# Performance work log

Hardware: AMD Instinct MI355X
Metric: run time of the kernel (lower is better)

## Reference

```python
import jax, jax.numpy as jnp
import numpy as np

B, M, L, HID, H, LAYERS = 16, 128, 512, 256, 4, 2
DH = HID // H  # 64 = head dim, also kernel_param dim


def _ln(x, g, b, eps=1e-5):
    mu = jnp.mean(x, axis=-1, keepdims=True)
    var = jnp.mean((x - mu) ** 2, axis=-1, keepdims=True)
    return (x - mu) / jnp.sqrt(var + eps) * g + b


def setup_inputs() -> dict:
    key = jax.random.key(0)
    ks = jax.random.split(key, 24)
    s = 0.05
    return {
        "ct_t": jax.random.uniform(ks[0], (B, M), jnp.float32),
        "ts_t": jax.random.uniform(ks[1], (B, L), jnp.float32),
        "ct_emb": jax.random.normal(ks[2], (B, M, HID), jnp.float32),
        "ts_emb": jax.random.normal(ks[3], (B, L, HID), jnp.float32),
        "kernel_param": jax.random.normal(ks[4], (DH,), jnp.float32),
        "ct_W": jax.random.normal(ks[5], (HID, HID), jnp.float32) * s,
        "ct_b": jnp.zeros((HID,), jnp.float32),
        "fW0": jax.random.normal(ks[6], (HID, HID), jnp.float32) * s,
        "fb0": jnp.zeros((HID,), jnp.float32),
        "fW1": jax.random.normal(ks[7], (HID, HID), jnp.float32) * s,
        "fb1": jnp.zeros((HID,), jnp.float32),
        "fW2": jax.random.normal(ks[8], (HID, HID), jnp.float32) * s,
        "fb2": jnp.zeros((HID,), jnp.float32),
        "f_ln_g": jnp.ones((HID,), jnp.float32),
        "f_ln_b": jnp.zeros((HID,), jnp.float32),
        "Wqkv": jax.random.normal(ks[9], (LAYERS, 3 * HID, HID), jnp.float32) * s,
        "bqkv": jnp.zeros((LAYERS, 3 * HID), jnp.float32),
        "Wo": jax.random.normal(ks[10], (LAYERS, HID, HID), jnp.float32) * s,
        "bo": jnp.zeros((LAYERS, HID), jnp.float32),
        "W1": jax.random.normal(ks[11], (LAYERS, 2 * HID, HID), jnp.float32) * s,
        "b1": jnp.zeros((LAYERS, 2 * HID), jnp.float32),
        "W2": jax.random.normal(ks[12], (LAYERS, HID, 2 * HID), jnp.float32) * s,
        "b2": jnp.zeros((LAYERS, HID), jnp.float32),
        "ln1_g": jnp.ones((LAYERS, HID), jnp.float32),
        "ln1_b": jnp.zeros((LAYERS, HID), jnp.float32),
        "ln2_g": jnp.ones((LAYERS, HID), jnp.float32),
        "ln2_b": jnp.zeros((LAYERS, HID), jnp.float32),
        "pred_W": jax.random.normal(ks[13], (1, HID), jnp.float32) * s,
        "pred_b": jnp.zeros((1,), jnp.float32),
    }


def reference(ct_t, ts_t, ct_emb, ts_emb, kernel_param, ct_W, ct_b,
              fW0, fb0, fW1, fb1, fW2, fb2, f_ln_g, f_ln_b,
              Wqkv, bqkv, Wo, bo, W1, b1, W2, b2,
              ln1_g, ln1_b, ln2_g, ln2_b, pred_W, pred_b):
    # --- TN tokenizer: multi-scale RBF kernel temporal fusion ---
    alpha = jax.nn.softplus(kernel_param)                       # [DH]  log(1+exp(p))
    ct_e = (jnp.einsum('bmd,ed->bme', ct_emb, ct_W) + ct_b)     # [B,M,HID]
    ct_e = ct_e.reshape(B, M, H, DH)
    diff = ct_t[:, :, None] - ts_t[:, None, :]                  # [B,M,L]
    norm = (diff * diff)[..., None]                             # [B,M,L,1]
    outs = []
    for s in range(H):                                          # fixed small loop over scales
        z = (-float(s)) * alpha * norm                          # [B,M,L,DH]
        w = jax.nn.logsumexp(z, axis=3, keepdims=True)          # [B,M,L,1]
        sim = jnp.exp(z - w)                                    # normalized kernel sims
        outs.append(jnp.einsum('bmnd,bmd->bnd', sim, ct_e[:, :, s, :]))  # scatter over ts events
    temp = jnp.concatenate(outs, axis=-1)                       # [B,L,HID]
    # --- Fusion module ---
    aux = jax.nn.elu(temp @ fW0.T + fb0 + ts_emb @ fW1.T + fb1)
    x = _ln(aux @ fW2.T + fb2 + ts_emb, f_ln_g, f_ln_b)         # [B,L,HID]
    # --- Transformer encoder (post-LN, gelu, no dropout at eval) ---
    inv_sqrt = 1.0 / np.sqrt(DH).astype(np.float32)
    for l in range(LAYERS):
        qkv = x @ Wqkv[l].T + bqkv[l]                           # [B,L,3*HID]
        q, k, v = jnp.split(qkv, 3, axis=-1)
        def heads(t):
            return t.reshape(B, L, H, DH).transpose(0, 2, 1, 3)
        q, k, v = heads(q), heads(k), heads(v)
        att = jax.nn.softmax(jnp.einsum('bhqd,bhkd->bhqk', q, k) * inv_sqrt, axis=-1)
        o = jnp.einsum('bhqk,bhkd->bhqd', att, v).transpose(0, 2, 1, 3).reshape(B, L, HID)
        x = _ln(x + o @ Wo[l].T + bo[l], ln1_g[l], ln1_b[l])
        ff = jax.nn.gelu(x @ W1[l].T + b1[l], approximate=False) @ W2[l].T + b2[l]
        x = _ln(x + ff, ln2_g[l], ln2_b[l])
    return x @ pred_W.T + pred_b                                # [B,L,1]
```

## Files before the change

### kernel.cpp

```cpp
#include <hip/hip_runtime.h>
#include <hip/hip_bf16.h>
#include <cstddef>

#define Bsz 16
#define Msz 128
#define Lsz 512
#define HIDs 256

typedef __attribute__((ext_vector_type(4))) float f32x4;
typedef __attribute__((ext_vector_type(8))) __bf16 bf16x8;
typedef __attribute__((ext_vector_type(8))) unsigned short ushort8;

#define CHEB_K 12
#define PI_F 3.14159265358979323846f

static __device__ inline unsigned short f2bf(float f) {
    __hip_bfloat16 h = __float2bfloat16(f);
    return *(unsigned short*)&h;
}
static __device__ inline float bf2f(unsigned short u) {
    return __builtin_bit_cast(float, (unsigned)u << 16);
}
static __device__ inline void gload16(const ushort* g, ushort* l) {
    __builtin_amdgcn_global_load_lds(
        (const __attribute__((address_space(1))) void*)g,
        (__attribute__((address_space(3))) void*)l, 16, 0, 0);
}

__global__ __launch_bounds__(256) void cvt_all_kernel(
    const float* __restrict__ ts_emb, const float* __restrict__ ct_emb,
    const float* __restrict__ ct_W, const float* __restrict__ fW0,
    const float* __restrict__ fW1, const float* __restrict__ fW2,
    const float* __restrict__ Wqkv, const float* __restrict__ Wo,
    const float* __restrict__ W1, const float* __restrict__ W2,
    ushort* __restrict__ Xcat, ushort* __restrict__ Wcat,
    ushort* __restrict__ cebin, ushort* __restrict__ wct,
    ushort* __restrict__ wf2, ushort* __restrict__ wqkv,
    ushort* __restrict__ wo, ushort* __restrict__ w1, ushort* __restrict__ w2)
{
    const unsigned u = blockIdx.x * 256u + threadIdx.x;
    const float* src; ushort* dst; unsigned rel;
    if (u < 262144u) {
        rel = u; src = ts_emb;
        dst = Xcat + ((size_t)(rel >> 5) * 512 + 256 + (rel & 31) * 8);
    } else if (u < 327680u) { rel = u - 262144u; src = ct_emb; dst = cebin + (size_t)rel * 8; }
    else if (u < 335872u) { rel = u - 327680u; src = ct_W; dst = wct + (size_t)rel * 8; }
    else if (u < 344064u) { rel = u - 335872u; src = fW0;
        dst = Wcat + ((size_t)(rel >> 5) * 512 + (rel & 31) * 8); }
    else if (u < 352256u) { rel = u - 344064u; src = fW1;
        dst = Wcat + ((size_t)(rel >> 5) * 512 + 256 + (rel & 31) * 8); }
    else if (u < 360448u) { rel = u - 352256u; src = fW2; dst = wf2 + (size_t)rel * 8; }
    else if (u < 409600u) { rel = u - 360448u; src = Wqkv; dst = wqkv + (size_t)rel * 8; }
    else if (u < 425984u) { rel = u - 409600u; src = Wo;  dst = wo + (size_t)rel * 8; }
    else if (u < 458752u) { rel = u - 425984u; src = W1;  dst = w1 + (size_t)rel * 8; }
    else                  { rel = u - 458752u; src = W2;  dst = w2 + (size_t)rel * 8; }
    float4 a = ((const float4*)src)[(size_t)rel * 2];
    float4 b = ((const float4*)src)[(size_t)rel * 2 + 1];
    ushort8 o;
    o[0] = f2bf(a.x); o[1] = f2bf(a.y); o[2] = f2bf(a.z); o[3] = f2bf(a.w);
    o[4] = f2bf(b.x); o[5] = f2bf(b.y); o[6] = f2bf(b.z); o[7] = f2bf(b.w);
    *(ushort8*)dst = o;
}

__global__ __launch_bounds__(256) void gemm_mfma_kernel(
    const ushort* __restrict__ X, const ushort* __restrict__ W,
    const float* __restrict__ bias, const float* __restrict__ bias2,
    float* __restrict__ Yf, ushort* __restrict__ Yb,
    int NR, int K, int OUT, int act)
{
    __shared__ ushort As[2][64 * 64];
    __shared__ ushort Bs[2][128 * 64];

    const int nbx = OUT >> 7;
    const int bx = blockIdx.x % nbx;
    const int by = blockIdx.x / nbx;
    const int r0 = by << 6, o0 = bx << 7;
    const int tid = threadIdx.x;
    const int w = tid >> 6;
    const int lane = tid & 63;
    const int wr = w >> 1, wc = w & 1;
    const int lr = lane & 15, lg = lane >> 4;

    const int grow = lane >> 3;
    const int gchunk = (lane & 7) ^ grow;

    unsigned aoff[2][2], boff[4][2];
    #pragma unroll
    for (int f = 0; f < 2; f++) {
        unsigned cc = (unsigned)((lg + 4 * f) ^ (lr & 7)) * 16u;
        #pragma unroll
        for (int m = 0; m < 2; m++)
            aoff[m][f] = (unsigned)(wr * 32 + m * 16 + lr) * 128u + cc;
        #pragma unroll
        for (int n = 0; n < 4; n++)
            boff[n][f] = (unsigned)(wc * 64 + n * 16 + lr) * 128u + cc;
    }

    f32x4 acc[2][4];
    #pragma unroll
    for (int m = 0; m < 2; m++)
        #pragma unroll
        for (int n = 0; n < 4; n++) acc[m][n] = (f32x4){0.f, 0.f, 0.f, 0.f};

    const int nk = K >> 6;

    auto stage = [&](int buf, int ks) {
        const int k0 = ks << 6;
        #pragma unroll
        for (int i = 0; i < 2; i++) {
            int row = w * 16 + i * 8 + grow;
            gload16(X + (size_t)(r0 + row) * K + k0 + gchunk * 8,
                    &As[buf][(w * 16 + i * 8) * 64]);
        }
        #pragma unroll
        for (int i = 0; i < 4; i++) {
            int row = w * 32 + i * 8 + grow;
            gload16(W + (size_t)(o0 + row) * K + k0 + gchunk * 8,
                    &Bs[buf][(w * 32 + i * 8) * 64]);
        }
    };

    stage(0, 0);
    __syncthreads();
    int cur = 0;
    for (int ks = 0; ks < nk; ks++) {
        if (ks + 1 < nk) stage(cur ^ 1, ks + 1);
        const char* Ab = (const char*)As[cur];
        const char* Bb = (const char*)Bs[cur];
        #pragma unroll
        for (int f = 0; f < 2; f++) {
            bf16x8 av[2], bv[4];
            #pragma unroll
            for (int m = 0; m < 2; m++)
                av[m] = *(const bf16x8*)(Ab + aoff[m][f]);
            #pragma unroll
            for (int n = 0; n < 4; n++)
                bv[n] = *(const bf16x8*)(Bb + boff[n][f]);
            #pragma unroll
            for (int m = 0; m < 2; m++)
                #pragma unroll
                for (int n = 0; n < 4; n++)
                    acc[m][n] = __builtin_amdgcn_mfma_f32_16x16x32_bf16(
                        av[m], bv[n], acc[m][n], 0, 0, 0);
        }
        __syncthreads();
        cur ^= 1;
    }

    const int ocol0 = o0 + wc * 64;
    float bn[4];
    #pragma unroll
    for (int n = 0; n < 4; n++) {
        int o = ocol0 + n * 16 + lr;
        bn[n] = bias[o] + (bias2 ? bias2[o] : 0.f);
    }

    #pragma unroll
    for (int m = 0; m < 2; m++) {
        #pragma unroll
        for (int p = 0; p < 4; p++) {
            int r = r0 + wr * 32 + m * 16 + 4 * lg + p;
            size_t rb = (size_t)r * OUT;
            #pragma unroll
            for (int n = 0; n < 4; n++) {
                int o = ocol0 + n * 16 + lr;
                float v = acc[m][n][p] + bn[n];
                if (act == 1)      v = (v > 0.f) ? v : (__expf(v) - 1.f);
                else if (act == 2) v = 0.5f * v * (1.f + erff(v * 0.70710678118654752f));
                if (Yf) Yf[rb + o] = v;
                if (Yb) Yb[rb + o] = f2bf(v);
            }
        }
    }
}

__global__ __launch_bounds__(256) void gemm_ln_kernel(
    const ushort* __restrict__ X, const ushort* __restrict__ W,
    const float* __restrict__ bias, const float* __restrict__ add,
    const float* __restrict__ lng, const float* __restrict__ lnb,
    float* __restrict__ Xf, ushort* __restrict__ Xb,
    const float* __restrict__ predW, const float* __restrict__ predb,
    float* __restrict__ pout, int K)
{
    __shared__ ushort As[2][32 * 64];
    __shared__ ushort Bs[2][256 * 64];
    __shared__ float redA[32][4];
    __shared__ float redB[32][4];

    const int r0 = blockIdx.x << 5;
    const int tid = threadIdx.x;
    const int w = tid >> 6;
    const int lane = tid & 63;
    const int lr = lane & 15, lg = lane >> 4;
    const int grow = lane >> 3;
    const int gchunk = (lane & 7) ^ grow;

    unsigned aoff[2][2], boff[4][2];
    #pragma unroll
    for (int f = 0; f < 2; f++) {
        unsigned cc = (unsigned)((lg + 4 * f) ^ (lr & 7)) * 16u;
        #pragma unroll
        for (int m = 0; m < 2; m++)
            aoff[m][f] = (unsigned)(m * 16 + lr) * 128u + cc;
        #pragma unroll
        for (int n = 0; n < 4; n++)
            boff[n][f] = (unsigned)(w * 64 + n * 16 + lr) * 128u + cc;
    }

    f32x4 acc[2][4];
    #pragma unroll
    for (int m = 0; m < 2; m++)
        #pragma unroll
        for (int n = 0; n < 4; n++) acc[m][n] = (f32x4){0.f, 0.f, 0.f, 0.f};

    const int nk = K >> 6;

    auto stage = [&](int buf, int ks) {
        const int k0 = ks << 6;
        gload16(X + (size_t)(r0 + w * 8 + grow) * K + k0 + gchunk * 8,
                &As[buf][(w * 8) * 64]);
        #pragma unroll
        for (int i = 0; i < 8; i++) {
            gload16(W + (size_t)(w * 64 + i * 8 + grow) * K + k0 + gchunk * 8,
                    &Bs[buf][(w * 64 + i * 8) * 64]);
        }
    };

    stage(0, 0);
    __syncthreads();
    int cur = 0;
    for (int ks = 0; ks < nk; ks++) {
        if (ks + 1 < nk) stage(cur ^ 1, ks + 1);
        const char* Ab = (const char*)As[cur];
        const char* Bb = (const char*)Bs[cur];
        #pragma unroll
        for (int f = 0; f < 2; f++) {
            bf16x8 av[2], bv[4];
            #pragma unroll
            for (int m = 0; m < 2; m++)
                av[m] = *(const bf16x8*)(Ab + aoff[m][f]);
            #pragma unroll
            for (int n = 0; n < 4; n++)
                bv[n] = *(const bf16x8*)(Bb + boff[n][f]);
            #pragma unroll
            for (int m = 0; m < 2; m++)
                #pragma unroll
                for (int n = 0; n < 4; n++)
                    acc[m][n] = __builtin_amdgcn_mfma_f32_16x16x32_bf16(
                        av[m], bv[n], acc[m][n], 0, 0, 0);
        }
        __syncthreads();
        cur ^= 1;
    }

    const int col0 = w * 64;
    float bn[4], gv[4], bv2[4], pwv[4];
    #pragma unroll
    for (int n = 0; n < 4; n++) {
        int o = col0 + n * 16 + lr;
        bn[n] = bias[o];
        gv[n] = lng[o];
        bv2[n] = lnb[o];
        pwv[n] = predW ? predW[o] : 0.f;
    }
    #pragma unroll
    for (int m = 0; m < 2; m++)
        #pragma unroll
        for (int p = 0; p < 4; p++) {
            int r = r0 + m * 16 + 4 * lg + p;
            size_t rb = (size_t)r * 256;
            #pragma unroll
            for (int n = 0; n < 4; n++)
                acc[m][n][p] += bn[n] + add[rb + col0 + n * 16 + lr];
        }

    #pragma unroll
    for (int m = 0; m < 2; m++)
        #pragma unroll
        for (int p = 0; p < 4; p++) {
            float s = acc[m][0][p] + acc[m][1][p] + acc[m][2][p] + acc[m][3][p];
            #pragma unroll
            for (int o = 1; o <= 8; o <<= 1) s += __shfl_xor(s, o);
            if (lr == 0) redA[m * 16 + 4 * lg + p][w] = s;
        }
    __syncthreads();
    float mu[2][4];
    #pragma unroll
    for (int m = 0; m < 2; m++)
        #pragma unroll
        for (int p = 0; p < 4; p++) {
            int row = m * 16 + 4 * lg + p;
            mu[m][p] = (redA[row][0] + redA[row][1] + redA[row][2] + redA[row][3])
                       * (1.f / 256.f);
        }

    #pragma unroll
    for (int m = 0; m < 2; m++)
        #pragma unroll
        for (int p = 0; p < 4; p++) {
            float q = 0.f;
            #pragma unroll
            for (int n = 0; n < 4; n++) {
                float dl = acc[m][n][p] - mu[m][p];
                q = fmaf(dl, dl, q);
            }
            #pragma unroll
            for (int o = 1; o <= 8; o <<= 1) q += __shfl_xor(q, o);
            if (lr == 0) redB[m * 16 + 4 * lg + p][w] = q;
        }
    __syncthreads();

    #pragma unroll
    for (int m = 0; m < 2; m++)
        #pragma unroll
        for (int p = 0; p < 4; p++) {
            int row = m * 16 + 4 * lg + p;
            float var = (redB[row][0] + redB[row][1] + redB[row][2] + redB[row][3])
                        * (1.f / 256.f);
            float rsig = rsqrtf(var + 1e-5f);
            int r = r0 + row;
            size_t rb = (size_t)r * 256;
            float pd = 0.f;
            #pragma unroll
            for (int n = 0; n < 4; n++) {
                int o = col0 + n * 16 + lr;
                float xn = (acc[m][n][p] - mu[m][p]) * rsig * gv[n] + bv2[n];
                if (Xf) Xf[rb + o] = xn;
                if (Xb) Xb[rb + o] = f2bf(xn);
                pd = fmaf(xn, pwv[n], pd);
            }
            if (predW) {
                #pragma unroll
                for (int o = 1; o <= 8; o <<= 1) pd += __shfl_xor(pd, o);
                if (lr == 0) redA[row][w] = pd;
            }
        }
    if (predW) {
        __syncthreads();
        if (tid < 32)
            pout[r0 + tid] = redA[tid][0] + redA[tid][1] + redA[tid][2]
                           + redA[tid][3] + predb[0];
    }
}

__global__ __launch_bounds__(256) void cheb_kernel(
    const float* __restrict__ kp, float* __restrict__ clut, float* __restrict__ cD)
{
    __shared__ float costab[CHEB_K][32];
    __shared__ float xq[32];
    __shared__ float alph[64];
    const int t = threadIdx.x;
    if (t < 64) {
        float p = kp[t];
        alph[t] = fmaxf(p, 0.f) + log1pf(__expf(-fabsf(p)));
    }
    #pragma unroll
    for (int i = 0; i < 2; i++) {
        int idx = i * 256 + t;
        if (idx < CHEB_K * 32) {
            int k = idx >> 5, q = idx & 31;
            float th = (q + 0.5f) * (PI_F / 32.f);
            costab[k][q] = __cosf((float)k * th);
        }
    }
    if (t < 32) xq[t] = 0.5f * (1.f + __cosf((t + 0.5f) * (PI_F / 32.f)));
    __syncthreads();

    if (t >= 192) return;
    const int d = t & 63, s1 = t >> 6;
    const float u = (float)(s1 + 1) * alph[d];
    float f[32];
    #pragma unroll
    for (int q = 0; q < 32; q++) f[q] = __expf(-u * xq[q]);
    #pragma unroll
    for (int k = 0; k < CHEB_K; k++) {
        float sum = 0.f;
        #pragma unroll
        for (int q = 0; q < 32; q++) sum = fmaf(f[q], costab[k][q], sum);
        float c = sum * ((k == 0 ? 1.f : 2.f) / 32.f);
        clut[s1 * (CHEB_K * 64) + k * 64 + d] = c;
        float sr = c;
        #pragma unroll
        for (int o = 1; o <= 32; o <<= 1) sr += __shfl_xor(sr, o, 64);
        if (d == 0) cD[s1 * CHEB_K + k] = sr;
    }
}

__global__ __launch_bounds__(256) void denom3_kernel(
    const float* __restrict__ ct_t, const float* __restrict__ ts_t,
    const float* __restrict__ cD, ushort* __restrict__ invW)
{
    __shared__ float cd[3][CHEB_K];
    const int tid = threadIdx.x;
    if (tid < 3 * CHEB_K) cd[tid / CHEB_K][tid % CHEB_K] = cD[tid];
    __syncthreads();

    const unsigned G = blockIdx.x * 256u + tid;
    const int b = G >> 16;
    const int n = (G >> 7) & 511;
    const int m = G & 127;

    float x = ct_t[b * Msz + m] - ts_t[b * Lsz + n];
    x = x * x;
    const float xi = 2.f * x - 1.f;
    const float xi2 = 2.f * xi;

    float t0 = 1.f, t1 = xi;
    float a1 = cd[0][0] + cd[0][1] * xi;
    float a2 = cd[1][0] + cd[1][1] * xi;
    float a3 = cd[2][0] + cd[2][1] * xi;
    #pragma unroll
    for (int k = 2; k < CHEB_K; k++) {
        float tn = fmaf(xi2, t1, -t0);
        a1 = fmaf(cd[0][k], tn, a1);
        a2 = fmaf(cd[1][k], tn, a2);
        a3 = fmaf(cd[2][k], tn, a3);
        t0 = t1; t1 = tn;
    }
    const size_t base = ((size_t)b * 3 * Lsz + n) * Msz + m;
    invW[base]                         = f2bf(1.f / a1);
    invW[base + (size_t)Lsz * Msz]     = f2bf(1.f / a2);
    invW[base + (size_t)2 * Lsz * Msz] = f2bf(1.f / a3);
}

__global__ __launch_bounds__(256) void tok3_kernel(
    const float* __restrict__ ct_t, const float* __restrict__ ts_t,
    const ushort* __restrict__ ceb, const ushort* __restrict__ invW,
    const float* __restrict__ clut, ushort* __restrict__ Xcat)
{
    const int bid = blockIdx.x;
    const int nt = bid & 7;
    const int s1 = (bid >> 3) % 3;
    const int b  = bid / 24;
    const int tid = threadIdx.x;
    const int w = tid >> 6, lane = tid & 63, g = lane >> 4, r = lane & 15;

    __shared__ ushort ceT[64][136];
    __shared__ float  cl[CHEB_K][64];
    __shared__ float  cts[128];

    #pragma unroll
    for (int i = 0; i < 8; i++) {
        int idx = i * 256 + tid;
        int m = idx >> 4, d4 = (idx & 15) << 2;
        const ushort* gp = ceb + (((size_t)b * 128 + m) << 8) + (s1 + 1) * 64 + d4;
        ushort4 v = *(const ushort4*)gp;
        ceT[d4 + 0][m] = v.x; ceT[d4 + 1][m] = v.y;
        ceT[d4 + 2][m] = v.z; ceT[d4 + 3][m] = v.w;
    }
    #pragma unroll
    for (int i = 0; i < 3; i++) {
        int idx = i * 256 + tid;
        cl[idx >> 6][idx & 63] = clut[s1 * (CHEB_K * 64) + idx];
    }
    if (tid < 128) cts[tid] = ct_t[b * 128 + tid];
    __syncthreads();

    const int nrow = nt * 64 + w * 16 + r;
    const float tsn = ts_t[b * 512 + nrow];

    float xi2v[4][8], Ta[4][8], Tb[4][8];
    #pragma unroll
    for (int t4 = 0; t4 < 4; t4++) {
        int m0 = 8 * g + 32 * t4;
        ushort8 iv = *(const ushort8*)&invW[((((size_t)b * 3 + s1) * 512 + nrow) << 7) + m0];
        #pragma unroll
        for (int j = 0; j < 8; j++) {
            float dfx = cts[m0 + j] - tsn;
            float x = dfx * dfx;
            float xi = 2.f * x - 1.f;
            float w0 = bf2f(iv[j]);
            xi2v[t4][j] = 2.f * xi;
            Ta[t4][j] = w0;
            Tb[t4][j] = w0 * xi;
        }
    }

    bf16x8 cef[4][4];
    #pragma unroll
    for (int db = 0; db < 4; db++)
        #pragma unroll
        for (int t4 = 0; t4 < 4; t4++)
            cef[db][t4] = *(const bf16x8*)&ceT[db * 16 + r][8 * g + 32 * t4];

    f32x4 acc[4];
    #pragma unroll
    for (int db = 0; db < 4; db++) acc[db] = (f32x4){0.f, 0.f, 0.f, 0.f};

    #pragma unroll
    for (int k = 0; k < CHEB_K; k++) {
        if (k >= 2) {
            #pragma unroll
            for (int t4 = 0; t4 < 4; t4++)
                #pragma unroll
                for (int j = 0; j < 8; j++) {
                    if (k & 1) Tb[t4][j] = fmaf(xi2v[t4][j], Ta[t4][j], -Tb[t4][j]);
                    else       Ta[t4][j] = fmaf(xi2v[t4][j], Tb[t4][j], -Ta[t4][j]);
                }
        }
        bf16x8 af[4];
        #pragma unroll
        for (int t4 = 0; t4 < 4; t4++) {
            ushort8 u;
            #pragma unroll
            for (int j = 0; j < 8; j++)
                u[j] = f2bf((k & 1) ? Tb[t4][j] : Ta[t4][j]);
            af[t4] = __builtin_bit_cast(bf16x8, u);
        }
        #pragma unroll
        for (int db = 0; db < 4; db++) {
            f32x4 gk = (f32x4){0.f, 0.f, 0.f, 0.f};
            #pragma unroll
            for (int t4 = 0; t4 < 4; t4++)
                gk = __builtin_amdgcn_mfma_f32_16x16x32_bf16(af[t4], cef[db][t4], gk, 0, 0, 0);
            float ck = cl[k][db * 16 + r];
            #pragma unroll
            for (int p = 0; p < 4; p++) acc[db][p] = fmaf(ck, gk[p], acc[db][p]);
        }
    }

    #pragma unroll
    for (int db = 0; db < 4; db++)
        #pragma unroll
        for (int p = 0; p < 4; p++) {
            int n_out = nt * 64 + w * 16 + 4 * g + p;
            Xcat[((size_t)b * 512 + n_out) * 512 + (s1 + 1) * 64 + db * 16 + r] =
                f2bf(acc[db][p]);
        }
}

__global__ __launch_bounds__(256) void bcast0_kernel(
    const ushort* __restrict__ ceb, ushort* __restrict__ Xcat)
{
    const int b = blockIdx.x;
    const int t = threadIdx.x;
    const int d = t & 63, q = t >> 6;
    float s = 0.f;
    #pragma unroll 8
    for (int i = 0; i < 32; i++) {
        int m = q * 32 + i;
        s += bf2f(ceb[(((size_t)b * 128 + m) << 8) + d]);
    }
    __shared__ float red[4][64];
    __shared__ ushort row[64];
    red[q][d] = s;
    __syncthreads();
    if (t < 64)
        row[t] = f2bf((red[0][t] + red[1][t] + red[2][t] + red[3][t]) * (1.f / 64.f));
    __syncthreads();
    #pragma unroll
    for (int i = 0; i < 16; i++) {
        int idx = i * 256 + t;
        int n = idx >> 3, j = idx & 7;
        *(ushort8*)&Xcat[((size_t)b * 512 + n) * 512 + j * 8] =
            *(const ushort8*)&row[j * 8];
    }
}

__global__ __launch_bounds__(256) void attn_mfma_kernel(
    const ushort* __restrict__ qkv, ushort* __restrict__ Ob)
{
    const int bid = blockIdx.x;
    const int qt = bid & 7;
    const int h  = (bid >> 3) & 3;
    const int b  = bid >> 5;
    const int t  = threadIdx.x;
    const int w  = t >> 6;
    const int lane = t & 63;
    const int g = lane >> 4;
    const int r = lane & 15;

    __shared__ ushort Ks[2][64][72];
    __shared__ ushort Vt[2][64][72];
    __shared__ float  Ps[4][16][65];

    const ushort* base = qkv + (size_t)b * Lsz * 768;
    const int q0 = qt * 64 + w * 16;

    bf16x8 qf[2];
    {
        const ushort* qp = base + (size_t)(q0 + r) * 768 + h * 64 + 8 * g;
        qf[0] = __builtin_bit_cast(bf16x8, *(const ushort8*)qp);
        qf[1] = __builtin_bit_cast(bf16x8, *(const ushort8*)(qp + 32));
    }

    f32x4 Ofr[4];
    #pragma unroll
    for (int dblk = 0; dblk < 4; dblk++) Ofr[dblk] = (f32x4){0.f, 0.f, 0.f, 0.f};
    float m_run[4] = {-1e30f, -1e30f, -1e30f, -1e30f};
    float l_run[4] = {0.f, 0.f, 0.f, 0.f};

    const int srow = t >> 2;
    const int sseg = t & 3;

    ushort8 pk0, pk1, pv0, pv1;
    auto gload_chunk = [&](int c) {
        const ushort* kr = base + (size_t)(c * 64 + srow) * 768 + 256 + h * 64 + sseg * 16;
        pk0 = *(const ushort8*)kr;
        pk1 = *(const ushort8*)(kr + 8);
        pv0 = *(const ushort8*)(kr + 256);
        pv1 = *(const ushort8*)(kr + 264);
    };
    auto write_chunk = [&](int buf) {
        *(ushort8*)&Ks[buf][srow][sseg * 16]     = pk0;
        *(ushort8*)&Ks[buf][srow][sseg * 16 + 8] = pk1;
        #pragma unroll
        for (int j = 0; j < 8; j++) {
            Vt[buf][sseg * 16 + j][srow]     = pv0[j];
            Vt[buf][sseg * 16 + 8 + j][srow] = pv1[j];
        }
    };

    gload_chunk(0);
    write_chunk(0);
    __syncthreads();
    int cur = 0;

    for (int c = 0; c < 8; c++) {
        if (c < 7) gload_chunk(c + 1);

        f32x4 sfr[4];
        #pragma unroll
        for (int s = 0; s < 4; s++) {
            f32x4 a2 = (f32x4){0.f, 0.f, 0.f, 0.f};
            #pragma unroll
            for (int f = 0; f < 2; f++) {
                bf16x8 kf = *(const bf16x8*)&Ks[cur][s * 16 + r][8 * g + 32 * f];
                a2 = __builtin_amdgcn_mfma_f32_16x16x32_bf16(qf[f], kf, a2, 0, 0, 0);
            }
            #pragma unroll
            for (int p = 0; p < 4; p++) a2[p] *= 0.125f;
            sfr[s] = a2;
        }

        #pragma unroll
        for (int p = 0; p < 4; p++) {
            float rm = fmaxf(fmaxf(sfr[0][p], sfr[1][p]), fmaxf(sfr[2][p], sfr[3][p]));
            #pragma unroll
            for (int o = 1; o <= 8; o <<= 1) rm = fmaxf(rm, __shfl_xor(rm, o));
            float mnew = fmaxf(m_run[p], rm);
            float sc = __expf(m_run[p] - mnew);
            m_run[p] = mnew;
            float rs = 0.f;
            #pragma unroll
            for (int s = 0; s < 4; s++) {
                float pv = __expf(sfr[s][p] - mnew);
                Ps[w][4 * g + p][s * 16 + r] = pv;
                rs += pv;
            }
            #pragma unroll
            for (int o = 1; o <= 8; o <<= 1) rs += __shfl_xor(rs, o);
            l_run[p] = l_run[p] * sc + rs;
            #pragma unroll
            for (int dblk = 0; dblk < 4; dblk++) Ofr[dblk][p] *= sc;
        }

        __asm__ volatile("s_waitcnt lgkmcnt(0)" ::: "memory");

        #pragma unroll
        for (int f = 0; f < 2; f++) {
            const float* pp = &Ps[w][r][8 * g + 32 * f];
            ushort8 ua;
            #pragma unroll
            for (int j = 0; j < 8; j++) ua[j] = f2bf(pp[j]);
            bf16x8 pa = __builtin_bit_cast(bf16x8, ua);
            #pragma unroll
            for (int dblk = 0; dblk < 4; dblk++) {
                bf16x8 vb = *(const bf16x8*)&Vt[cur][dblk * 16 + r][32 * f + 8 * g];
                Ofr[dblk] = __builtin_amdgcn_mfma_f32_16x16x32_bf16(
                    pa, vb, Ofr[dblk], 0, 0, 0);
            }
        }

        if (c < 7) write_chunk(cur ^ 1);
        __syncthreads();
        cur ^= 1;
    }

    #pragma unroll
    for (int dblk = 0; dblk < 4; dblk++) {
        #pragma unroll
        for (int p = 0; p < 4; p++) {
            int row = q0 + 4 * g + p;
            Ob[(size_t)(b * Lsz + row) * HIDs + h * 64 + dblk * 16 + r] =
                f2bf(Ofr[dblk][p] / l_run[p]);
        }
    }
}

extern "C" void kernel_launch(void* const* d_in, const int* in_sizes, int n_in,
                              void* d_out, int out_size, void* d_ws, size_t ws_size,
                              hipStream_t stream)
{
    (void)in_sizes; (void)n_in; (void)out_size; (void)ws_size;

    const float* ct_t   = (const float*)d_in[0];
    const float* ts_t   = (const float*)d_in[1];
    const float* ct_emb = (const float*)d_in[2];
    const float* ts_emb = (const float*)d_in[3];
    const float* kp     = (const float*)d_in[4];
    const float* ct_W   = (const float*)d_in[5];
    const float* ct_b   = (const float*)d_in[6];
    const float* fW0    = (const float*)d_in[7];
    const float* fb0    = (const float*)d_in[8];
    const float* fW1    = (const float*)d_in[9];
    const float* fb1    = (const float*)d_in[10];
    const float* fW2    = (const float*)d_in[11];
    const float* fb2    = (const float*)d_in[12];
    const float* f_ln_g = (const float*)d_in[13];
    const float* f_ln_b = (const float*)d_in[14];
    const float* Wqkv   = (const float*)d_in[15];
    const float* bqkv   = (const float*)d_in[16];
    const float* Wo     = (const float*)d_in[17];
    const float* bo     = (const float*)d_in[18];
    const float* W1     = (const float*)d_in[19];
    const float* b1     = (const float*)d_in[20];
    const float* W2     = (const float*)d_in[21];
    const float* b2     = (const float*)d_in[22];
    const float* ln1_g  = (const float*)d_in[23];
    const float* ln1_b  = (const float*)d_in[24];
    const float* ln2_g  = (const float*)d_in[25];
    const float* ln2_b  = (const float*)d_in[26];
    const float* pred_W = (const float*)d_in[27];
    const float* pred_b = (const float*)d_in[28];

    ushort* wsb = (ushort*)d_ws;
    ushort* invW  = wsb;
    ushort* auxbf = wsb;
    ushort* qkvbf = wsb;
    ushort* ff1bf = wsb;
    ushort* Xcat  = wsb + 12582912;
    ushort* Wcat  = wsb + 16777216;
    ushort* cebin = wsb + 16908288;
    ushort* cebout= wsb + 17432576;
    ushort* wct   = wsb + 17956864;
    ushort* wf2   = wsb + 18022400;
    ushort* wqkv  = wsb + 18087936;
    ushort* wo    = wsb + 18481152;
    ushort* w1    = wsb + 18612224;
    ushort* w2    = wsb + 18874368;
    ushort* xbf   = wsb + 19136512;
    ushort* obf   = wsb + 21233664;
    float*  wsf   = (float*)d_ws;
    float*  xbuf  = wsf + 11665408;
    float*  clut  = wsf + 13762560;
    float*  cDp   = wsf + 13764864;

    const int NRts = Bsz * Lsz;
    const int NRct = Bsz * Msz;
    auto grid = [](int nr, int out) { return dim3((unsigned)((nr >> 6) * (out >> 7))); };

    cvt_all_kernel<<<dim3(1920), 256, 0, stream>>>(
        ts_emb, ct_emb, ct_W, fW0, fW1, fW2, Wqkv, Wo, W1, W2,
        Xcat, Wcat, cebin, wct, wf2, wqkv, wo, w1, w2);

    gemm_mfma_kernel<<<grid(NRct, 256), 256, 0, stream>>>(
        cebin, wct, ct_b, nullptr, nullptr, cebout, NRct, 256, 256, 0);
    cheb_kernel<<<dim3(1), 256, 0, stream>>>(kp, clut, cDp);
    denom3_kernel<<<dim3(Bsz * Msz * Lsz / 256), 256, 0, stream>>>(ct_t, ts_t, cDp, invW);
    tok3_kernel<<<dim3(384), 256, 0, stream>>>(ct_t, ts_t, cebout, invW, clut, Xcat);
    bcast0_kernel<<<dim3(Bsz), 256, 0, stream>>>(cebout, Xcat);

    gemm_mfma_kernel<<<grid(NRts, 256), 256, 0, stream>>>(
        Xcat, Wcat, fb0, fb1, nullptr, auxbf, NRts, 512, 256, 1);
    gemm_ln_kernel<<<dim3(NRts / 32), 256, 0, stream>>>(
        auxbf, wf2, fb2, ts_emb, f_ln_g, f_ln_b, xbuf, xbf,
        nullptr, nullptr, nullptr, 256);

    for (int l = 0; l < 2; l++) {
        gemm_mfma_kernel<<<grid(NRts, 768), 256, 0, stream>>>(
            xbf, wqkv + (size_t)l * 196608, bqkv + l * 768, nullptr,
            nullptr, qkvbf, NRts, 256, 768, 0);
        attn_mfma_kernel<<<dim3(512), 256, 0, stream>>>(qkvbf, obf);
        gemm_ln_kernel<<<dim3(NRts / 32), 256, 0, stream>>>(
            obf, wo + (size_t)l * 65536, bo + l * 256, xbuf,
            ln1_g + l * 256, ln1_b + l * 256, xbuf, xbf,
            nullptr, nullptr, nullptr, 256);
        gemm_mfma_kernel<<<grid(NRts, 512), 256, 0, stream>>>(
            xbf, w1 + (size_t)l * 131072, b1 + l * 512, nullptr,
            nullptr, ff1bf, NRts, 256, 512, 2);
        if (l == 0) {
            gemm_ln_kernel<<<dim3(NRts / 32), 256, 0, stream>>>(
                ff1bf, w2 + (size_t)l * 131072, b2 + l * 256, xbuf,
                ln2_g + l * 256, ln2_b + l * 256, xbuf, xbf,
                nullptr, nullptr, nullptr, 512);
        } else {
            gemm_ln_kernel<<<dim3(NRts / 32), 256, 0, stream>>>(
                ff1bf, w2 + (size_t)l * 131072, b2 + l * 256, xbuf,
                ln2_g + l * 256, ln2_b + l * 256, nullptr, nullptr,
                pred_W, pred_b, (float*)d_out, 512);
        }
    }
}
```

Measured before the change: 218.4 us.

## Merge prep kernels, fuse token mixing with broadcast, shrink LN-GEMM row tile

```diff
diff --git a/kernel.cpp b/kernel.cpp
--- a/kernel.cpp
+++ b/kernel.cpp
@@ -25,322 +25,6 @@
     __builtin_amdgcn_global_load_lds(
         (const __attribute__((address_space(1))) void*)g,
         (__attribute__((address_space(3))) void*)l, 16, 0, 0);
-}
-
-__global__ __launch_bounds__(256) void cvt_all_kernel(
-    const float* __restrict__ ts_emb, const float* __restrict__ ct_emb,
-    const float* __restrict__ ct_W, const float* __restrict__ fW0,
-    const float* __restrict__ fW1, const float* __restrict__ fW2,
-    const float* __restrict__ Wqkv, const float* __restrict__ Wo,
-    const float* __restrict__ W1, const float* __restrict__ W2,
-    ushort* __restrict__ Xcat, ushort* __restrict__ Wcat,
-    ushort* __restrict__ cebin, ushort* __restrict__ wct,
-    ushort* __restrict__ wf2, ushort* __restrict__ wqkv,
-    ushort* __restrict__ wo, ushort* __restrict__ w1, ushort* __restrict__ w2)
-{
-    const unsigned u = blockIdx.x * 256u + threadIdx.x;
-    const float* src; ushort* dst; unsigned rel;
-    if (u < 262144u) {
-        rel = u; src = ts_emb;
-        dst = Xcat + ((size_t)(rel >> 5) * 512 + 256 + (rel & 31) * 8);
-    } else if (u < 327680u) { rel = u - 262144u; src = ct_emb; dst = cebin + (size_t)rel * 8; }
-    else if (u < 335872u) { rel = u - 327680u; src = ct_W; dst = wct + (size_t)rel * 8; }
-    else if (u < 344064u) { rel = u - 335872u; src = fW0;
-        dst = Wcat + ((size_t)(rel >> 5) * 512 + (rel & 31) * 8); }
-    else if (u < 352256u) { rel = u - 344064u; src = fW1;
-        dst = Wcat + ((size_t)(rel >> 5) * 512 + 256 + (rel & 31) * 8); }
-    else if (u < 360448u) { rel = u - 352256u; src = fW2; dst = wf2 + (size_t)rel * 8; }
-    else if (u < 409600u) { rel = u - 360448u; src = Wqkv; dst = wqkv + (size_t)rel * 8; }
-    else if (u < 425984u) { rel = u - 409600u; src = Wo;  dst = wo + (size_t)rel * 8; }
-    else if (u < 458752u) { rel = u - 425984u; src = W1;  dst = w1 + (size_t)rel * 8; }
-    else                  { rel = u - 458752u; src = W2;  dst = w2 + (size_t)rel * 8; }
-    float4 a = ((const float4*)src)[(size_t)rel * 2];
-    float4 b = ((const float4*)src)[(size_t)rel * 2 + 1];
-    ushort8 o;
-    o[0] = f2bf(a.x); o[1] = f2bf(a.y); o[2] = f2bf(a.z); o[3] = f2bf(a.w);
-    o[4] = f2bf(b.x); o[5] = f2bf(b.y); o[6] = f2bf(b.z); o[7] = f2bf(b.w);
-    *(ushort8*)dst = o;
-}
-
-__global__ __launch_bounds__(256) void gemm_mfma_kernel(
-    const ushort* __restrict__ X, const ushort* __restrict__ W,
-    const float* __restrict__ bias, const float* __restrict__ bias2,
-    float* __restrict__ Yf, ushort* __restrict__ Yb,
-    int NR, int K, int OUT, int act)
-{
-    __shared__ ushort As[2][64 * 64];
-    __shared__ ushort Bs[2][128 * 64];
-
-    const int nbx = OUT >> 7;
-    const int bx = blockIdx.x % nbx;
-    const int by = blockIdx.x / nbx;
-    const int r0 = by << 6, o0 = bx << 7;
-    const int tid = threadIdx.x;
-    const int w = tid >> 6;
-    const int lane = tid & 63;
-    const int wr = w >> 1, wc = w & 1;
-    const int lr = lane & 15, lg = lane >> 4;
-
-    const int grow = lane >> 3;
-    const int gchunk = (lane & 7) ^ grow;
-
-    unsigned aoff[2][2], boff[4][2];
-    #pragma unroll
-    for (int f = 0; f < 2; f++) {
-        unsigned cc = (unsigned)((lg + 4 * f) ^ (lr & 7)) * 16u;
-        #pragma unroll
-        for (int m = 0; m < 2; m++)
-            aoff[m][f] = (unsigned)(wr * 32 + m * 16 + lr) * 128u + cc;
-        #pragma unroll
-        for (int n = 0; n < 4; n++)
-            boff[n][f] = (unsigned)(wc * 64 + n * 16 + lr) * 128u + cc;
-    }
-
-    f32x4 acc[2][4];
-    #pragma unroll
-    for (int m = 0; m < 2; m++)
-        #pragma unroll
-        for (int n = 0; n < 4; n++) acc[m][n] = (f32x4){0.f, 0.f, 0.f, 0.f};
-
-    const int nk = K >> 6;
-
-    auto stage = [&](int buf, int ks) {
-        const int k0 = ks << 6;
-        #pragma unroll
-        for (int i = 0; i < 2; i++) {
-            int row = w * 16 + i * 8 + grow;
-            gload16(X + (size_t)(r0 + row) * K + k0 + gchunk * 8,
-                    &As[buf][(w * 16 + i * 8) * 64]);
-        }
-        #pragma unroll
-        for (int i = 0; i < 4; i++) {
-            int row = w * 32 + i * 8 + grow;
-            gload16(W + (size_t)(o0 + row) * K + k0 + gchunk * 8,
-                    &Bs[buf][(w * 32 + i * 8) * 64]);
-        }
-    };
-
-    stage(0, 0);
-    __syncthreads();
-    int cur = 0;
-    for (int ks = 0; ks < nk; ks++) {
-        if (ks + 1 < nk) stage(cur ^ 1, ks + 1);
-        const char* Ab = (const char*)As[cur];
-        const char* Bb = (const char*)Bs[cur];
-        #pragma unroll
-        for (int f = 0; f < 2; f++) {
-            bf16x8 av[2], bv[4];
-            #pragma unroll
-            for (int m = 0; m < 2; m++)
-                av[m] = *(const bf16x8*)(Ab + aoff[m][f]);
-            #pragma unroll
-            for (int n = 0; n < 4; n++)
-                bv[n] = *(const bf16x8*)(Bb + boff[n][f]);
-            #pragma unroll
-            for (int m = 0; m < 2; m++)
-                #pragma unroll
-                for (int n = 0; n < 4; n++)
-                    acc[m][n] = __builtin_amdgcn_mfma_f32_16x16x32_bf16(
-                        av[m], bv[n], acc[m][n], 0, 0, 0);
-        }
-        __syncthreads();
-        cur ^= 1;
-    }
-
-    const int ocol0 = o0 + wc * 64;
-    float bn[4];
-    #pragma unroll
-    for (int n = 0; n < 4; n++) {
-        int o = ocol0 + n * 16 + lr;
-        bn[n] = bias[o] + (bias2 ? bias2[o] : 0.f);
-    }
-
-    #pragma unroll
-    for (int m = 0; m < 2; m++) {
-        #pragma unroll
-        for (int p = 0; p < 4; p++) {
-            int r = r0 + wr * 32 + m * 16 + 4 * lg + p;
-            size_t rb = (size_t)r * OUT;
-            #pragma unroll
-            for (int n = 0; n < 4; n++) {
-                int o = ocol0 + n * 16 + lr;
-                float v = acc[m][n][p] + bn[n];
-                if (act == 1)      v = (v > 0.f) ? v : (__expf(v) - 1.f);
-                else if (act == 2) v = 0.5f * v * (1.f + erff(v * 0.70710678118654752f));
-                if (Yf) Yf[rb + o] = v;
-                if (Yb) Yb[rb + o] = f2bf(v);
-            }
-        }
-    }
-}
-
-__global__ __launch_bounds__(256) void gemm_ln_kernel(
-    const ushort* __restrict__ X, const ushort* __restrict__ W,
-    const float* __restrict__ bias, const float* __restrict__ add,
-    const float* __restrict__ lng, const float* __restrict__ lnb,
-    float* __restrict__ Xf, ushort* __restrict__ Xb,
-    const float* __restrict__ predW, const float* __restrict__ predb,
-    float* __restrict__ pout, int K)
-{
-    __shared__ ushort As[2][32 * 64];
-    __shared__ ushort Bs[2][256 * 64];
-    __shared__ float redA[32][4];
-    __shared__ float redB[32][4];
-
-    const int r0 = blockIdx.x << 5;
-    const int tid = threadIdx.x;
-    const int w = tid >> 6;
-    const int lane = tid & 63;
-    const int lr = lane & 15, lg = lane >> 4;
-    const int grow = lane >> 3;
-    const int gchunk = (lane & 7) ^ grow;
-
-    unsigned aoff[2][2], boff[4][2];
-    #pragma unroll
-    for (int f = 0; f < 2; f++) {
-        unsigned cc = (unsigned)((lg + 4 * f) ^ (lr & 7)) * 16u;
-        #pragma unroll
-        for (int m = 0; m < 2; m++)
-            aoff[m][f] = (unsigned)(m * 16 + lr) * 128u + cc;
-        #pragma unroll
-        for (int n = 0; n < 4; n++)
-            boff[n][f] = (unsigned)(w * 64 + n * 16 + lr) * 128u + cc;
-    }
-
-    f32x4 acc[2][4];
-    #pragma unroll
-    for (int m = 0; m < 2; m++)
-        #pragma unroll
-        for (int n = 0; n < 4; n++) acc[m][n] = (f32x4){0.f, 0.f, 0.f, 0.f};
-
-    const int nk = K >> 6;
-
-    auto stage = [&](int buf, int ks) {
-        const int k0 = ks << 6;
-        gload16(X + (size_t)(r0 + w * 8 + grow) * K + k0 + gchunk * 8,
-                &As[buf][(w * 8) * 64]);
-        #pragma unroll
-        for (int i = 0; i < 8; i++) {
-            gload16(W + (size_t)(w * 64 + i * 8 + grow) * K + k0 + gchunk * 8,
-                    &Bs[buf][(w * 64 + i * 8) * 64]);
-        }
-    };
-
-    stage(0, 0);
-    __syncthreads();
-    int cur = 0;
-    for (int ks = 0; ks < nk; ks++) {
-        if (ks + 1 < nk) stage(cur ^ 1, ks + 1);
-        const char* Ab = (const char*)As[cur];
-        const char* Bb = (const char*)Bs[cur];
-        #pragma unroll
-        for (int f = 0; f < 2; f++) {
-            bf16x8 av[2], bv[4];
-            #pragma unroll
-            for (int m = 0; m < 2; m++)
-                av[m] = *(const bf16x8*)(Ab + aoff[m][f]);
-            #pragma unroll
-            for (int n = 0; n < 4; n++)
-                bv[n] = *(const bf16x8*)(Bb + boff[n][f]);
-            #pragma unroll
-            for (int m = 0; m < 2; m++)
-                #pragma unroll
-                for (int n = 0; n < 4; n++)
-                    acc[m][n] = __builtin_amdgcn_mfma_f32_16x16x32_bf16(
-                        av[m], bv[n], acc[m][n], 0, 0, 0);
-        }
-        __syncthreads();
-        cur ^= 1;
-    }
-
-    const int col0 = w * 64;
-    float bn[4], gv[4], bv2[4], pwv[4];
-    #pragma unroll
-    for (int n = 0; n < 4; n++) {
-        int o = col0 + n * 16 + lr;
-        bn[n] = bias[o];
-        gv[n] = lng[o];
-        bv2[n] = lnb[o];
-        pwv[n] = predW ? predW[o] : 0.f;
-    }
-    #pragma unroll
-    for (int m = 0; m < 2; m++)
-        #pragma unroll
-        for (int p = 0; p < 4; p++) {
-            int r = r0 + m * 16 + 4 * lg + p;
-            size_t rb = (size_t)r * 256;
-            #pragma unroll
-            for (int n = 0; n < 4; n++)
-                acc[m][n][p] += bn[n] + add[rb + col0 + n * 16 + lr];
-        }
-
-    #pragma unroll
-    for (int m = 0; m < 2; m++)
-        #pragma unroll
-        for (int p = 0; p < 4; p++) {
-            float s = acc[m][0][p] + acc[m][1][p] + acc[m][2][p] + acc[m][3][p];
-            #pragma unroll
-            for (int o = 1; o <= 8; o <<= 1) s += __shfl_xor(s, o);
-            if (lr == 0) redA[m * 16 + 4 * lg + p][w] = s;
-        }
-    __syncthreads();
-    float mu[2][4];
-    #pragma unroll
-    for (int m = 0; m < 2; m++)
-        #pragma unroll
-        for (int p = 0; p < 4; p++) {
-            int row = m * 16 + 4 * lg + p;
-            mu[m][p] = (redA[row][0] + redA[row][1] + redA[row][2] + redA[row][3])
-                       * (1.f / 256.f);
-        }
-
-    #pragma unroll
-    for (int m = 0; m < 2; m++)
-        #pragma unroll
-        for (int p = 0; p < 4; p++) {
-            float q = 0.f;
-            #pragma unroll
-            for (int n = 0; n < 4; n++) {
-                float dl = acc[m][n][p] - mu[m][p];
-                q = fmaf(dl, dl, q);
-            }
-            #pragma unroll
-            for (int o = 1; o <= 8; o <<= 1) q += __shfl_xor(q, o);
-            if (lr == 0) redB[m * 16 + 4 * lg + p][w] = q;
-        }
-    __syncthreads();
-
-    #pragma unroll
-    for (int m = 0; m < 2; m++)
-        #pragma unroll
-        for (int p = 0; p < 4; p++) {
-            int row = m * 16 + 4 * lg + p;
-            float var = (redB[row][0] + redB[row][1] + redB[row][2] + redB[row][3])
-                        * (1.f / 256.f);
-            float rsig = rsqrtf(var + 1e-5f);
-            int r = r0 + row;
-            size_t rb = (size_t)r * 256;
-            float pd = 0.f;
-            #pragma unroll
-            for (int n = 0; n < 4; n++) {
-                int o = col0 + n * 16 + lr;
-                float xn = (acc[m][n][p] - mu[m][p]) * rsig * gv[n] + bv2[n];
-                if (Xf) Xf[rb + o] = xn;
-                if (Xb) Xb[rb + o] = f2bf(xn);
-                pd = fmaf(xn, pwv[n], pd);
-            }
-            if (predW) {
-                #pragma unroll
-                for (int o = 1; o <= 8; o <<= 1) pd += __shfl_xor(pd, o);
-                if (lr == 0) redA[row][w] = pd;
-            }
-        }
-    if (predW) {
-        __syncthreads();
-        if (tid < 32)
-            pout[r0 + tid] = redA[tid][0] + redA[tid][1] + redA[tid][2]
-                           + redA[tid][3] + predb[0];
-    }
 }
 
 __global__ __launch_bounds__(256) void cheb_kernel(
@@ -386,174 +70,471 @@
     }
 }
 
-__global__ __launch_bounds__(256) void denom3_kernel(
+__global__ __launch_bounds__(256) void prep_kernel(
+    const float* __restrict__ ts_emb, const float* __restrict__ ct_emb,
+    const float* __restrict__ ct_W, const float* __restrict__ fW0,
+    const float* __restrict__ fW1, const float* __restrict__ fW2,
+    const float* __restrict__ Wqkv, const float* __restrict__ Wo,
+    const float* __restrict__ W1, const float* __restrict__ W2,
+    ushort* __restrict__ Xcat, ushort* __restrict__ Wcat,
+    ushort* __restrict__ cebin, ushort* __restrict__ wct,
+    ushort* __restrict__ wf2, ushort* __restrict__ wqkv,
+    ushort* __restrict__ wo, ushort* __restrict__ w1, ushort* __restrict__ w2,
     const float* __restrict__ ct_t, const float* __restrict__ ts_t,
     const float* __restrict__ cD, ushort* __restrict__ invW)
 {
-    __shared__ float cd[3][CHEB_K];
+    const int bid = blockIdx.x;
     const int tid = threadIdx.x;
-    if (tid < 3 * CHEB_K) cd[tid / CHEB_K][tid % CHEB_K] = cD[tid];
+
+    if (bid < 1920) {
+        const unsigned u = bid * 256u + tid;
+        const float* src; ushort* dst; unsigned rel;
+        if (u < 262144u) {
+            rel = u; src = ts_emb;
+            dst = Xcat + ((size_t)(rel >> 5) * 512 + 256 + (rel & 31) * 8);
+        } else if (u < 327680u) { rel = u - 262144u; src = ct_emb; dst = cebin + (size_t)rel * 8; }
+        else if (u < 335872u) { rel = u - 327680u; src = ct_W; dst = wct + (size_t)rel * 8; }
+        else if (u < 344064u) { rel = u - 335872u; src = fW0;
+            dst = Wcat + ((size_t)(rel >> 5) * 512 + (rel & 31) * 8); }
+        else if (u < 352256u) { rel = u - 344064u; src = fW1;
+            dst = Wcat + ((size_t)(rel >> 5) * 512 + 256 + (rel & 31) * 8); }
+        else if (u < 360448u) { rel = u - 352256u; src = fW2; dst = wf2 + (size_t)rel * 8; }
+        else if (u < 409600u) { rel = u - 360448u; src = Wqkv; dst = wqkv + (size_t)rel * 8; }
+        else if (u < 425984u) { rel = u - 409600u; src = Wo;  dst = wo + (size_t)rel * 8; }
+        else if (u < 458752u) { rel = u - 425984u; src = W1;  dst = w1 + (size_t)rel * 8; }
+        else                  { rel = u - 458752u; src = W2;  dst = w2 + (size_t)rel * 8; }
+        float4 a = ((const float4*)src)[(size_t)rel * 2];
+        float4 b = ((const float4*)src)[(size_t)rel * 2 + 1];
+        ushort8 o;
+        o[0] = f2bf(a.x); o[1] = f2bf(a.y); o[2] = f2bf(a.z); o[3] = f2bf(a.w);
+        o[4] = f2bf(b.x); o[5] = f2bf(b.y); o[6] = f2bf(b.z); o[7] = f2bf(b.w);
+        *(ushort8*)dst = o;
+    } else {
+        __shared__ float cd[3][CHEB_K];
+        if (tid < 3 * CHEB_K) cd[tid / CHEB_K][tid % CHEB_K] = cD[tid];
+        __syncthreads();
+
+        const unsigned G = (bid - 1920) * 256u + tid;
+        const int b = G >> 16;
+        const int n = (G >> 7) & 511;
+        const int m = G & 127;
+
+        float x = ct_t[b * Msz + m] - ts_t[b * Lsz + n];
+        x = x * x;
+        const float xi = 2.f * x - 1.f;
+        const float xi2 = 2.f * xi;
+
+        float t0 = 1.f, t1 = xi;
+        float a1 = cd[0][0] + cd[0][1] * xi;
+        float a2 = cd[1][0] + cd[1][1] * xi;
+        float a3 = cd[2][0] + cd[2][1] * xi;
+        #pragma unroll
+        for (int k = 2; k < CHEB_K; k++) {
+            float tn = fmaf(xi2, t1, -t0);
+            a1 = fmaf(cd[0][k], tn, a1);
+            a2 = fmaf(cd[1][k], tn, a2);
+            a3 = fmaf(cd[2][k], tn, a3);
+            t0 = t1; t1 = tn;
+        }
+        const size_t base = ((size_t)b * 3 * Lsz + n) * Msz + m;
+        invW[base]                         = f2bf(1.f / a1);
+        invW[base + (size_t)Lsz * Msz]     = f2bf(1.f / a2);
+        invW[base + (size_t)2 * Lsz * Msz] = f2bf(1.f / a3);
+    }
+}
+
+__global__ __launch_bounds__(256) void gemm_mfma_kernel(
+    const ushort* __restrict__ X, const ushort* __restrict__ W,
+    const float* __restrict__ bias, const float* __restrict__ bias2,
+    float* __restrict__ Yf, ushort* __restrict__ Yb,
+    int NR, int K, int OUT, int act)
+{
+    __shared__ ushort As[2][64 * 64];
+    __shared__ ushort Bs[2][128 * 64];
+
+    const int nbx = OUT >> 7;
+    const int bx = blockIdx.x % nbx;
+    const int by = blockIdx.x / nbx;
+    const int r0 = by << 6, o0 = bx << 7;
+    const int tid = threadIdx.x;
+    const int w = tid >> 6;
+    const int lane = tid & 63;
+    const int wr = w >> 1, wc = w & 1;
+    const int lr = lane & 15, lg = lane >> 4;
+
+    const int grow = lane >> 3;
+    const int gchunk = (lane & 7) ^ grow;
+
+    unsigned aoff[2][2], boff[4][2];
+    #pragma unroll
+    for (int f = 0; f < 2; f++) {
+        unsigned cc = (unsigned)((lg + 4 * f) ^ (lr & 7)) * 16u;
+        #pragma unroll
+        for (int m = 0; m < 2; m++)
+            aoff[m][f] = (unsigned)(wr * 32 + m * 16 + lr) * 128u + cc;
+        #pragma unroll
+        for (int n = 0; n < 4; n++)
+            boff[n][f] = (unsigned)(wc * 64 + n * 16 + lr) * 128u + cc;
+    }
+
+    f32x4 acc[2][4];
+    #pragma unroll
+    for (int m = 0; m < 2; m++)
+        #pragma unroll
+        for (int n = 0; n < 4; n++) acc[m][n] = (f32x4){0.f, 0.f, 0.f, 0.f};
+
+    const int nk = K >> 6;
+
+    auto stage = [&](int buf, int ks) {
+        const int k0 = ks << 6;
+        #pragma unroll
+        for (int i = 0; i < 2; i++) {
+            int row = w * 16 + i * 8 + grow;
+            gload16(X + (size_t)(r0 + row) * K + k0 + gchunk * 8,
+                    &As[buf][(w * 16 + i * 8) * 64]);
+        }
+        #pragma unroll
+        for (int i = 0; i < 4; i++) {
+            int row = w * 32 + i * 8 + grow;
+            gload16(W + (size_t)(o0 + row) * K + k0 + gchunk * 8,
+                    &Bs[buf][(w * 32 + i * 8) * 64]);
+        }
+    };
+
+    stage(0, 0);
     __syncthreads();
-
-    const unsigned G = blockIdx.x * 256u + tid;
-    const int b = G >> 16;
-    const int n = (G >> 7) & 511;
-    const int m = G & 127;
-
-    float x = ct_t[b * Msz + m] - ts_t[b * Lsz + n];
-    x = x * x;
-    const float xi = 2.f * x - 1.f;
-    const float xi2 = 2.f * xi;
-
-    float t0 = 1.f, t1 = xi;
-    float a1 = cd[0][0] + cd[0][1] * xi;
-    float a2 = cd[1][0] + cd[1][1] * xi;
-    float a3 = cd[2][0] + cd[2][1] * xi;
-    #pragma unroll
-    for (int k = 2; k < CHEB_K; k++) {
-        float tn = fmaf(xi2, t1, -t0);
-        a1 = fmaf(cd[0][k], tn, a1);
-        a2 = fmaf(cd[1][k], tn, a2);
-        a3 = fmaf(cd[2][k], tn, a3);
-        t0 = t1; t1 = tn;
-    }
-    const size_t base = ((size_t)b * 3 * Lsz + n) * Msz + m;
-    invW[base]                         = f2bf(1.f / a1);
-    invW[base + (size_t)Lsz * Msz]     = f2bf(1.f / a2);
-    invW[base + (size_t)2 * Lsz * Msz] = f2bf(1.f / a3);
-}
-
-__global__ __launch_bounds__(256) void tok3_kernel(
+    int cur = 0;
+    for (int ks = 0; ks < nk; ks++) {
+        if (ks + 1 < nk) stage(cur ^ 1, ks + 1);
+        const char* Ab = (const char*)As[cur];
+        const char* Bb = (const char*)Bs[cur];
+        #pragma unroll
+        for (int f = 0; f < 2; f++) {
+            bf16x8 av[2], bv[4];
+            #pragma unroll
+            for (int m = 0; m < 2; m++)
+                av[m] = *(const bf16x8*)(Ab + aoff[m][f]);
+            #pragma unroll
+            for (int n = 0; n < 4; n++)
+                bv[n] = *(const bf16x8*)(Bb + boff[n][f]);
+            #pragma unroll
+            for (int m = 0; m < 2; m++)
+                #pragma unroll
+                for (int n = 0; n < 4; n++)
+                    acc[m][n] = __builtin_amdgcn_mfma_f32_16x16x32_bf16(
+                        av[m], bv[n], acc[m][n], 0, 0, 0);
+        }
+        __syncthreads();
+        cur ^= 1;
+    }
+
+    const int ocol0 = o0 + wc * 64;
+    float bn[4];
+    #pragma unroll
+    for (int n = 0; n < 4; n++) {
+        int o = ocol0 + n * 16 + lr;
+        bn[n] = bias[o] + (bias2 ? bias2[o] : 0.f);
+    }
+
+    #pragma unroll
+    for (int m = 0; m < 2; m++) {
+        #pragma unroll
+        for (int p = 0; p < 4; p++) {
+            int r = r0 + wr * 32 + m * 16 + 4 * lg + p;
+            size_t rb = (size_t)r * OUT;
+            #pragma unroll
+            for (int n = 0; n < 4; n++) {
+                int o = ocol0 + n * 16 + lr;
+                float v = acc[m][n][p] + bn[n];
+                if (act == 1)      v = (v > 0.f) ? v : (__expf(v) - 1.f);
+                else if (act == 2) v = 0.5f * v * (1.f + erff(v * 0.70710678118654752f));
+                if (Yf) Yf[rb + o] = v;
+                if (Yb) Yb[rb + o] = f2bf(v);
+            }
+        }
+    }
+}
+
+__global__ __launch_bounds__(256) void gemm_ln_kernel(
+    const ushort* __restrict__ X, const ushort* __restrict__ W,
+    const float* __restrict__ bias, const float* __restrict__ add,
+    const float* __restrict__ lng, const float* __restrict__ lnb,
+    float* __restrict__ Xf, ushort* __restrict__ Xb,
+    const float* __restrict__ predW, const float* __restrict__ predb,
+    float* __restrict__ pout, int K)
+{
+    __shared__ ushort As[2][16 * 64];
+    __shared__ ushort Bs[2][256 * 64];
+    __shared__ float redA[16][4];
+    __shared__ float redB[16][4];
+
+    const int r0 = blockIdx.x << 4;
+    const int tid = threadIdx.x;
+    const int w = tid >> 6;
+    const int lane = tid & 63;
+    const int lr = lane & 15, lg = lane >> 4;
+    const int grow = lane >> 3;
+    const int gchunk = (lane & 7) ^ grow;
+
+    unsigned aoff[2], boff[4][2];
+    #pragma unroll
+    for (int f = 0; f < 2; f++) {
+        unsigned cc = (unsigned)((lg + 4 * f) ^ (lr & 7)) * 16u;
+        aoff[f] = (unsigned)lr * 128u + cc;
+        #pragma unroll
+        for (int n = 0; n < 4; n++)
+            boff[n][f] = (unsigned)(w * 64 + n * 16 + lr) * 128u + cc;
+    }
+
+    f32x4 acc[4];
+    #pragma unroll
+    for (int n = 0; n < 4; n++) acc[n] = (f32x4){0.f, 0.f, 0.f, 0.f};
+
+    const int nk = K >> 6;
+
+    auto stage = [&](int buf, int ks) {
+        const int k0 = ks << 6;
+        if (w < 2)
+            gload16(X + (size_t)(r0 + w * 8 + grow) * K + k0 + gchunk * 8,
+                    &As[buf][(w * 8) * 64]);
+        #pragma unroll
+        for (int i = 0; i < 8; i++) {
+            gload16(W + (size_t)(w * 64 + i * 8 + grow) * K + k0 + gchunk * 8,
+                    &Bs[buf][(w * 64 + i * 8) * 64]);
+        }
+    };
+
+    stage(0, 0);
+    __syncthreads();
+    int cur = 0;
+    for (int ks = 0; ks < nk; ks++) {
+        if (ks + 1 < nk) stage(cur ^ 1, ks + 1);
+        const char* Ab = (const char*)As[cur];
+        const char* Bb = (const char*)Bs[cur];
+        #pragma unroll
+        for (int f = 0; f < 2; f++) {
+            bf16x8 av = *(const bf16x8*)(Ab + aoff[f]);
+            #pragma unroll
+            for (int n = 0; n < 4; n++) {
+                bf16x8 bv = *(const bf16x8*)(Bb + boff[n][f]);
+                acc[n] = __builtin_amdgcn_mfma_f32_16x16x32_bf16(
+                    av, bv, acc[n], 0, 0, 0);
+            }
+        }
+        __syncthreads();
+        cur ^= 1;
+    }
+
+    const int col0 = w * 64;
+    float bn[4], gv[4], bv2[4], pwv[4];
+    #pragma unroll
+    for (int n = 0; n < 4; n++) {
+        int o = col0 + n * 16 + lr;
+        bn[n] = bias[o];
+        gv[n] = lng[o];
+        bv2[n] = lnb[o];
+        pwv[n] = predW ? predW[o] : 0.f;
+    }
+    #pragma unroll
+    for (int p = 0; p < 4; p++) {
+        int r = r0 + 4 * lg + p;
+        size_t rb = (size_t)r * 256;
+        #pragma unroll
+        for (int n = 0; n < 4; n++)
+            acc[n][p] += bn[n] + add[rb + col0 + n * 16 + lr];
+    }
+
+    #pragma unroll
+    for (int p = 0; p < 4; p++) {
+        float s = acc[0][p] + acc[1][p] + acc[2][p] + acc[3][p];
+        #pragma unroll
+        for (int o = 1; o <= 8; o <<= 1) s += __shfl_xor(s, o);
+        if (lr == 0) redA[4 * lg + p][w] = s;
+    }
+    __syncthreads();
+    float mu[4];
+    #pragma unroll
+    for (int p = 0; p < 4; p++) {
+        int row = 4 * lg + p;
+        mu[p] = (redA[row][0] + redA[row][1] + redA[row][2] + redA[row][3])
+                * (1.f / 256.f);
+    }
+
+    #pragma unroll
+    for (int p = 0; p < 4; p++) {
+        float q = 0.f;
+        #pragma unroll
+        for (int n = 0; n < 4; n++) {
+            float dl = acc[n][p] - mu[p];
+            q = fmaf(dl, dl, q);
+        }
+        #pragma unroll
+        for (int o = 1; o <= 8; o <<= 1) q += __shfl_xor(q, o);
+        if (lr == 0) redB[4 * lg + p][w] = q;
+    }
+    __syncthreads();
+
+    #pragma unroll
+    for (int p = 0; p < 4; p++) {
+        int row = 4 * lg + p;
+        float var = (redB[row][0] + redB[row][1] + redB[row][2] + redB[row][3])
+                    * (1.f / 256.f);
+        float rsig = rsqrtf(var + 1e-5f);
+        int r = r0 + row;
+        size_t rb = (size_t)r * 256;
+        float pd = 0.f;
+        #pragma unroll
+        for (int n = 0; n < 4; n++) {
+            int o = col0 + n * 16 + lr;
+            float xn = (acc[n][p] - mu[p]) * rsig * gv[n] + bv2[n];
+            if (Xf) Xf[rb + o] = xn;
+            if (Xb) Xb[rb + o] = f2bf(xn);
+            pd = fmaf(xn, pwv[n], pd);
+        }
+        if (predW) {
+            #pragma unroll
+            for (int o = 1; o <= 8; o <<= 1) pd += __shfl_xor(pd, o);
+            if (lr == 0) redA[row][w] = pd;
+        }
+    }
+    if (predW) {
+        __syncthreads();
+        if (tid < 16)
+            pout[r0 + tid] = redA[tid][0] + redA[tid][1] + redA[tid][2]
+                           + redA[tid][3] + predb[0];
+    }
+}
+
+__global__ __launch_bounds__(256) void tokmix_kernel(
     const float* __restrict__ ct_t, const float* __restrict__ ts_t,
     const ushort* __restrict__ ceb, const ushort* __restrict__ invW,
     const float* __restrict__ clut, ushort* __restrict__ Xcat)
 {
     const int bid = blockIdx.x;
-    const int nt = bid & 7;
-    const int s1 = (bid >> 3) % 3;
-    const int b  = bid / 24;
     const int tid = threadIdx.x;
-    const int w = tid >> 6, lane = tid & 63, g = lane >> 4, r = lane & 15;
-
-    __shared__ ushort ceT[64][136];
-    __shared__ float  cl[CHEB_K][64];
-    __shared__ float  cts[128];
-
-    #pragma unroll
-    for (int i = 0; i < 8; i++) {
-        int idx = i * 256 + tid;
-        int m = idx >> 4, d4 = (idx & 15) << 2;
-        const ushort* gp = ceb + (((size_t)b * 128 + m) << 8) + (s1 + 1) * 64 + d4;
-        ushort4 v = *(const ushort4*)gp;
-        ceT[d4 + 0][m] = v.x; ceT[d4 + 1][m] = v.y;
-        ceT[d4 + 2][m] = v.z; ceT[d4 + 3][m] = v.w;
-    }
-    #pragma unroll
-    for (int i = 0; i < 3; i++) {
-        int idx = i * 256 + tid;
-        cl[idx >> 6][idx & 63] = clut[s1 * (CHEB_K * 64) + idx];
-    }
-    if (tid < 128) cts[tid] = ct_t[b * 128 + tid];
-    __syncthreads();
-
-    const int nrow = nt * 64 + w * 16 + r;
-    const float tsn = ts_t[b * 512 + nrow];
-
-    float xi2v[4][8], Ta[4][8], Tb[4][8];
-    #pragma unroll
-    for (int t4 = 0; t4 < 4; t4++) {
-        int m0 = 8 * g + 32 * t4;
-        ushort8 iv = *(const ushort8*)&invW[((((size_t)b * 3 + s1) * 512 + nrow) << 7) + m0];
-        #pragma unroll
-        for (int j = 0; j < 8; j++) {
-            float dfx = cts[m0 + j] - tsn;
-            float x = dfx * dfx;
-            float xi = 2.f * x - 1.f;
-            float w0 = bf2f(iv[j]);
-            xi2v[t4][j] = 2.f * xi;
-            Ta[t4][j] = w0;
-            Tb[t4][j] = w0 * xi;
-        }
-    }
-
-    bf16x8 cef[4][4];
-    #pragma unroll
-    for (int db = 0; db < 4; db++)
-        #pragma unroll
-        for (int t4 = 0; t4 < 4; t4++)
-            cef[db][t4] = *(const bf16x8*)&ceT[db * 16 + r][8 * g + 32 * t4];
-
-    f32x4 acc[4];
-    #pragma unroll
-    for (int db = 0; db < 4; db++) acc[db] = (f32x4){0.f, 0.f, 0.f, 0.f};
-
-    #pragma unroll
-    for (int k = 0; k < CHEB_K; k++) {
-        if (k >= 2) {
+
+    if (bid < 384) {
+        const int nt = bid & 7;
+        const int s1 = (bid >> 3) % 3;
+        const int b  = bid / 24;
+        const int w = tid >> 6, lane = tid & 63, g = lane >> 4, r = lane & 15;
+
+        __shared__ ushort ceT[64][136];
+        __shared__ float  cl[CHEB_K][64];
+        __shared__ float  cts[128];
+
+        #pragma unroll
+        for (int i = 0; i < 8; i++) {
+            int idx = i * 256 + tid;
+            int m = idx >> 4, d4 = (idx & 15) << 2;
+            const ushort* gp = ceb + (((size_t)b * 128 + m) << 8) + (s1 + 1) * 64 + d4;
+            ushort4 v = *(const ushort4*)gp;
+            ceT[d4 + 0][m] = v.x; ceT[d4 + 1][m] = v.y;
+            ceT[d4 + 2][m] = v.z; ceT[d4 + 3][m] = v.w;
+        }
+        #pragma unroll
+        for (int i = 0; i < 3; i++) {
+            int idx = i * 256 + tid;
+            cl[idx >> 6][idx & 63] = clut[s1 * (CHEB_K * 64) + idx];
+        }
+        if (tid < 128) cts[tid] = ct_t[b * 128 + tid];
+        __syncthreads();
+
+        const int nrow = nt * 64 + w * 16 + r;
+        const float tsn = ts_t[b * 512 + nrow];
+
+        float xi2v[4][8], Ta[4][8], Tb[4][8];
+        #pragma unroll
+        for (int t4 = 0; t4 < 4; t4++) {
+            int m0 = 8 * g + 32 * t4;
+            ushort8 iv = *(const ushort8*)&invW[((((size_t)b * 3 + s1) * 512 + nrow) << 7) + m0];
+            #pragma unroll
+            for (int j = 0; j < 8; j++) {
+                float dfx = cts[m0 + j] - tsn;
+                float x = dfx * dfx;
+                float xi = 2.f * x - 1.f;
+                float w0 = bf2f(iv[j]);
+                xi2v[t4][j] = 2.f * xi;
+                Ta[t4][j] = w0;
+                Tb[t4][j] = w0 * xi;
+            }
+        }
+
+        bf16x8 cef[4][4];
+        #pragma unroll
+        for (int db = 0; db < 4; db++)
             #pragma unroll
             for (int t4 = 0; t4 < 4; t4++)
+                cef[db][t4] = *(const bf16x8*)&ceT[db * 16 + r][8 * g + 32 * t4];
+
+        f32x4 acc[4];
+        #pragma unroll
+        for (int db = 0; db < 4; db++) acc[db] = (f32x4){0.f, 0.f, 0.f, 0.f};
+
+        #pragma unroll
+        for (int k = 0; k < CHEB_K; k++) {
+            if (k >= 2) {
                 #pragma unroll
-                for (int j = 0; j < 8; j++) {
-                    if (k & 1) Tb[t4][j] = fmaf(xi2v[t4][j], Ta[t4][j], -Tb[t4][j]);
-                    else       Ta[t4][j] = fmaf(xi2v[t4][j], Tb[t4][j], -Ta[t4][j]);
-                }
-        }
-        bf16x8 af[4];
-        #pragma unroll
-        for (int t4 = 0; t4 < 4; t4++) {
-            ushort8 u;
-            #pragma unroll
-            for (int j = 0; j < 8; j++)
-                u[j] = f2bf((k & 1) ? Tb[t4][j] : Ta[t4][j]);
-            af[t4] = __builtin_bit_cast(bf16x8, u);
-        }
-        #pragma unroll
-        for (int db = 0; db < 4; db++) {
-            f32x4 gk = (f32x4){0.f, 0.f, 0.f, 0.f};
-            #pragma unroll
-            for (int t4 = 0; t4 < 4; t4++)
-                gk = __builtin_amdgcn_mfma_f32_16x16x32_bf16(af[t4], cef[db][t4], gk, 0, 0, 0);
-            float ck = cl[k][db * 16 + r];
-            #pragma unroll
-            for (int p = 0; p < 4; p++) acc[db][p] = fmaf(ck, gk[p], acc[db][p]);
-        }
-    }
-
-    #pragma unroll
-    for (int db = 0; db < 4; db++)
-        #pragma unroll
-        for (int p = 0; p < 4; p++) {
-            int n_out = nt * 64 + w * 16 + 4 * g + p;
-            Xcat[((size_t)b * 512 + n_out) * 512 + (s1 + 1) * 64 + db * 16 + r] =
-                f2bf(acc[db][p]);
-        }
-}
-
-__global__ __launch_bounds__(256) void bcast0_kernel(
-    const ushort* __restrict__ ceb, ushort* __restrict__ Xcat)
-{
-    const int b = blockIdx.x;
-    const int t = threadIdx.x;
-    const int d = t & 63, q = t >> 6;
-    float s = 0.f;
-    #pragma unroll 8
-    for (int i = 0; i < 32; i++) {
-        int m = q * 32 + i;
-        s += bf2f(ceb[(((size_t)b * 128 + m) << 8) + d]);
-    }
-    __shared__ float red[4][64];
-    __shared__ ushort row[64];
-    red[q][d] = s;
-    __syncthreads();
-    if (t < 64)
-        row[t] = f2bf((red[0][t] + red[1][t] + red[2][t] + red[3][t]) * (1.f / 64.f));
-    __syncthreads();
-    #pragma unroll
-    for (int i = 0; i < 16; i++) {
-        int idx = i * 256 + t;
-        int n = idx >> 3, j = idx & 7;
-        *(ushort8*)&Xcat[((size_t)b * 512 + n) * 512 + j * 8] =
-            *(const ushort8*)&row[j * 8];
+                for (int t4 = 0; t4 < 4; t4++)
+                    #pragma unroll
+                    for (int j = 0; j < 8; j++) {
+                        if (k & 1) Tb[t4][j] = fmaf(xi2v[t4][j], Ta[t4][j], -Tb[t4][j]);
+                        else       Ta[t4][j] = fmaf(xi2v[t4][j], Tb[t4][j], -Ta[t4][j]);
+                    }
+            }
+            bf16x8 af[4];
+            #pragma unroll
+            for (int t4 = 0; t4 < 4; t4++) {
+                ushort8 u;
+                #pragma unroll
+                for (int j = 0; j < 8; j++)
+                    u[j] = f2bf((k & 1) ? Tb[t4][j] : Ta[t4][j]);
+                af[t4] = __builtin_bit_cast(bf16x8, u);
+            }
+            #pragma unroll
+            for (int db = 0; db < 4; db++) {
+                f32x4 gk = (f32x4){0.f, 0.f, 0.f, 0.f};
+                #pragma unroll
+                for (int t4 = 0; t4 < 4; t4++)
+                    gk = __builtin_amdgcn_mfma_f32_16x16x32_bf16(af[t4], cef[db][t4], gk, 0, 0, 0);
+                float ck = cl[k][db * 16 + r];
+                #pragma unroll
+                for (int p = 0; p < 4; p++) acc[db][p] = fmaf(ck, gk[p], acc[db][p]);
+            }
+        }
+
+        #pragma unroll
+        for (int db = 0; db < 4; db++)
+            #pragma unroll
+            for (int p = 0; p < 4; p++) {
+                int n_out = nt * 64 + w * 16 + 4 * g + p;
+                Xcat[((size_t)b * 512 + n_out) * 512 + (s1 + 1) * 64 + db * 16 + r] =
+                    f2bf(acc[db][p]);
+            }
+    } else {
+        const int b = bid - 384;
+        const int d = tid & 63, q = tid >> 6;
+        float s = 0.f;
+        #pragma unroll 8
+        for (int i = 0; i < 32; i++) {
+            int m = q * 32 + i;
+            s += bf2f(ceb[(((size_t)b * 128 + m) << 8) + d]);
+        }
+        __shared__ float red0[4][64];
+        __shared__ ushort row0[64];
+        red0[q][d] = s;
+        __syncthreads();
+        if (tid < 64)
+            row0[tid] = f2bf((red0[0][tid] + red0[1][tid] + red0[2][tid] + red0[3][tid])
+                             * (1.f / 64.f));
+        __syncthreads();
+        #pragma unroll
+        for (int i = 0; i < 16; i++) {
+            int idx = i * 256 + tid;
+            int n = idx >> 3, j = idx & 7;
+            *(ushort8*)&Xcat[((size_t)b * 512 + n) * 512 + j * 8] =
+                *(const ushort8*)&row0[j * 8];
+        }
     }
 }
 
@@ -570,8 +551,8 @@
     const int g = lane >> 4;
     const int r = lane & 15;
 
-    __shared__ ushort Ks[2][64][72];
-    __shared__ ushort Vt[2][64][72];
+    __shared__ ushort Ks[64][72];
+    __shared__ ushort Vt[64][72];
     __shared__ float  Ps[4][16][65];
 
     const ushort* base = qkv + (size_t)b * Lsz * 768;
@@ -601,20 +582,19 @@
         pv0 = *(const ushort8*)(kr + 256);
         pv1 = *(const ushort8*)(kr + 264);
     };
-    auto write_chunk = [&](int buf) {
-        *(ushort8*)&Ks[buf][srow][sseg * 16]     = pk0;
-        *(ushort8*)&Ks[buf][srow][sseg * 16 + 8] = pk1;
+    auto write_chunk = [&]() {
+        *(ushort8*)&Ks[srow][sseg * 16]     = pk0;
+        *(ushort8*)&Ks[srow][sseg * 16 + 8] = pk1;
         #pragma unroll
         for (int j = 0; j < 8; j++) {
-            Vt[buf][sseg * 16 + j][srow]     = pv0[j];
-            Vt[buf][sseg * 16 + 8 + j][srow] = pv1[j];
+            Vt[sseg * 16 + j][srow]     = pv0[j];
+            Vt[sseg * 16 + 8 + j][srow] = pv1[j];
         }
     };
 
     gload_chunk(0);
-    write_chunk(0);
+    write_chunk();
     __syncthreads();
-    int cur = 0;
 
     for (int c = 0; c < 8; c++) {
         if (c < 7) gload_chunk(c + 1);
@@ -625,7 +605,7 @@
             f32x4 a2 = (f32x4){0.f, 0.f, 0.f, 0.f};
             #pragma unroll
             for (int f = 0; f < 2; f++) {
-                bf16x8 kf = *(const bf16x8*)&Ks[cur][s * 16 + r][8 * g + 32 * f];
+                bf16x8 kf = *(const bf16x8*)&Ks[s * 16 + r][8 * g + 32 * f];
                 a2 = __builtin_amdgcn_mfma_f32_16x16x32_bf16(qf[f], kf, a2, 0, 0, 0);
             }
             #pragma unroll
@@ -666,15 +646,17 @@
             bf16x8 pa = __builtin_bit_cast(bf16x8, ua);
             #pragma unroll
             for (int dblk = 0; dblk < 4; dblk++) {
-                bf16x8 vb = *(const bf16x8*)&Vt[cur][dblk * 16 + r][32 * f + 8 * g];
+                bf16x8 vb = *(const bf16x8*)&Vt[dblk * 16 + r][32 * f + 8 * g];
                 Ofr[dblk] = __builtin_amdgcn_mfma_f32_16x16x32_bf16(
                     pa, vb, Ofr[dblk], 0, 0, 0);
             }
         }
 
-        if (c < 7) write_chunk(cur ^ 1);
         __syncthreads();
-        cur ^= 1;
+        if (c < 7) {
+            write_chunk();
+            __syncthreads();
+        }
     }
 
     #pragma unroll
@@ -750,20 +732,19 @@
     const int NRct = Bsz * Msz;
     auto grid = [](int nr, int out) { return dim3((unsigned)((nr >> 6) * (out >> 7))); };
 
-    cvt_all_kernel<<<dim3(1920), 256, 0, stream>>>(
+    cheb_kernel<<<dim3(1), 256, 0, stream>>>(kp, clut, cDp);
+    prep_kernel<<<dim3(1920 + 4096), 256, 0, stream>>>(
         ts_emb, ct_emb, ct_W, fW0, fW1, fW2, Wqkv, Wo, W1, W2,
-        Xcat, Wcat, cebin, wct, wf2, wqkv, wo, w1, w2);
+        Xcat, Wcat, cebin, wct, wf2, wqkv, wo, w1, w2,
+        ct_t, ts_t, cDp, invW);
 
     gemm_mfma_kernel<<<grid(NRct, 256), 256, 0, stream>>>(
         cebin, wct, ct_b, nullptr, nullptr, cebout, NRct, 256, 256, 0);
-    cheb_kernel<<<dim3(1), 256, 0, stream>>>(kp, clut, cDp);
-    denom3_kernel<<<dim3(Bsz * Msz * Lsz / 256), 256, 0, stream>>>(ct_t, ts_t, cDp, invW);
-    tok3_kernel<<<dim3(384), 256, 0, stream>>>(ct_t, ts_t, cebout, invW, clut, Xcat);
-    bcast0_kernel<<<dim3(Bsz), 256, 0, stream>>>(cebout, Xcat);
+    tokmix_kernel<<<dim3(400), 256, 0, stream>>>(ct_t, ts_t, cebout, invW, clut, Xcat);
 
     gemm_mfma_kernel<<<grid(NRts, 256), 256, 0, stream>>>(
         Xcat, Wcat, fb0, fb1, nullptr, auxbf, NRts, 512, 256, 1);
-    gemm_ln_kernel<<<dim3(NRts / 32), 256, 0, stream>>>(
+    gemm_ln_kernel<<<dim3(NRts / 16), 256, 0, stream>>>(
         auxbf, wf2, fb2, ts_emb, f_ln_g, f_ln_b, xbuf, xbf,
         nullptr, nullptr, nullptr, 256);
 
@@ -772,7 +753,7 @@
             xbf, wqkv + (size_t)l * 196608, bqkv + l * 768, nullptr,
             nullptr, qkvbf, NRts, 256, 768, 0);
         attn_mfma_kernel<<<dim3(512), 256, 0, stream>>>(qkvbf, obf);
-        gemm_ln_kernel<<<dim3(NRts / 32), 256, 0, stream>>>(
+        gemm_ln_kernel<<<dim3(NRts / 16), 256, 0, stream>>>(
             obf, wo + (size_t)l * 65536, bo + l * 256, xbuf,
             ln1_g + l * 256, ln1_b + l * 256, xbuf, xbf,
             nullptr, nullptr, nullptr, 256);
@@ -780,12 +761,12 @@
             xbf, w1 + (size_t)l * 131072, b1 + l * 512, nullptr,
             nullptr, ff1bf, NRts, 256, 512, 2);
         if (l == 0) {
-            gemm_ln_kernel<<<dim3(NRts / 32), 256, 0, stream>>>(
+            gemm_ln_kernel<<<dim3(NRts / 16), 256, 0, stream>>>(
                 ff1bf, w2 + (size_t)l * 131072, b2 + l * 256, xbuf,
                 ln2_g + l * 256, ln2_b + l * 256, xbuf, xbf,
                 nullptr, nullptr, nullptr, 512);
         } else {
-            gemm_ln_kernel<<<dim3(NRts / 32), 256, 0, stream>>>(
+            gemm_ln_kernel<<<dim3(NRts / 16), 256, 0, stream>>>(
                 ff1bf, w2 + (size_t)l * 131072, b2 + l * 256, xbuf,
                 ln2_g + l * 256, ln2_b + l * 256, nullptr, nullptr,
                 pred_W, pred_b, (float*)d_out, 512);
```

Measured after the change: 207.0 us. 1.06x faster.
